# Kernel tuning notes

Measured on AMD Instinct MI355X. Metric: run time of the kernel, lower is better.

The kernel has to match this reference:

```python
import jax, jax.numpy as jnp
import numpy as np

B, T, DIM = 4, 1024, 1024
HEADS, DH = 16, 64
MEM, CMEM, RATIO = 1024, 256, 4
KV = CMEM + MEM + T  # 2304
TOTAL_MEM = MEM + CMEM  # 1280
NEG = -np.finfo(np.float32).max


def shift(x):
    # Faithful port of the pad/flatten/reshape relative-position shift trick.
    b, h, i, j = x.shape
    x = jnp.concatenate([x, jnp.zeros((b, h, i, i), x.dtype)], axis=-1)  # [b,h,i,i+j]
    l = i + j - 1
    x = x.reshape(b, h, i * (i + j))
    pad = (-x.shape[-1]) % l
    x = jnp.pad(x, ((0, 0), (0, 0), (0, pad)))
    x = x.reshape(b, h, -1, l)
    return x[:, :, :i, i - 1:]  # [b,h,i,j]


def setup_inputs() -> dict:
    key = jax.random.key(0)
    ks = jax.random.split(key, 10)
    s = 0.02
    return {
        "x": jax.random.normal(ks[0], (B, T, DIM), jnp.float32),
        "mem": jax.random.normal(ks[1], (B, MEM, DIM), jnp.float32),
        "cmem": jax.random.normal(ks[2], (B, CMEM, DIM), jnp.float32),
        "pos_emb": jax.random.normal(ks[3], (HEADS, KV, DH), jnp.float32),
        "input_mask": jnp.ones((B, T), bool),
        "Wq": jax.random.normal(ks[4], (DIM, DIM), jnp.float32) * s,
        "Wkv": jax.random.normal(ks[5], (2 * DIM, DIM), jnp.float32) * s,
        "Wout": jax.random.normal(ks[6], (DIM, DIM), jnp.float32) * s,
        "bout": jnp.zeros((DIM,), jnp.float32),
        "conv_w": jax.random.normal(ks[7], (DIM, DIM, RATIO), jnp.float32) * s,
        "conv_b": jnp.zeros((DIM,), jnp.float32),
    }


def reference(x, mem, cmem, pos_emb, input_mask, Wq, Wkv, Wout, bout, conv_w, conv_b):
    b, t, e = x.shape
    scale = DH ** -0.5

    q = x @ Wq.T                                             # [b,t,e]
    kv_input = jnp.concatenate([cmem, mem, x], axis=1)       # [b,kv,e]
    kv_len = kv_input.shape[1]
    kv = kv_input @ Wkv.T                                    # [b,kv,2e]
    k, v = jnp.split(kv, 2, axis=-1)

    def mh(z):
        return z.reshape(z.shape[0], z.shape[1], HEADS, DH).transpose(0, 2, 1, 3)

    qh, kh, vh = mh(q), mh(k), mh(v)                         # [b,h,*,dh]

    dots = jnp.einsum('bhid,bhjd->bhij', qh, kh) * scale     # [b,h,t,kv]

    pe = pos_emb[:, -kv_len:].astype(qh.dtype)               # [h,kv,dh]
    pos_dots = shift(jnp.einsum('bhid,hjd->bhij', qh, pe) * scale)
    dots = dots + pos_dots

    # input mask (padded True over mem+cmem positions)
    m = input_mask[:, None, :, None] & input_mask[:, None, None, :]  # [b,1,t,t]
    m = jnp.pad(m, ((0, 0), (0, 0), (0, 0), (TOTAL_MEM, 0)), constant_values=True)
    dots = jnp.where(m, dots, NEG)

    # causal mask shifted by total memory length
    causal = jnp.triu(jnp.ones((t, t + TOTAL_MEM), bool), k=1 + TOTAL_MEM)
    dots = jnp.where(causal[None, None], NEG, dots)

    attn = jax.nn.softmax(dots, axis=-1)
    out = jnp.einsum('bhij,bhjd->bhid', attn, vh)
    out = out.transpose(0, 2, 1, 3).reshape(b, t, e)
    logits = out @ Wout.T + bout

    # memory update (eval path, calc_memory=True)
    queue = jnp.concatenate([mem, x], axis=1)                # [b,mem+t,e]
    new_mem = queue[:, -MEM:]
    old_mem = jax.lax.stop_gradient(queue[:, :-MEM])         # [b,t,e], t % RATIO == 0
    comp = jax.lax.conv_general_dilated(
        old_mem.transpose(0, 2, 1), conv_w, (RATIO,), 'VALID',
        dimension_numbers=('NCH', 'OIH', 'NCH')) + conv_b[None, :, None]
    comp = comp.transpose(0, 2, 1)                           # [b,t//RATIO,e]
    new_cmem = jnp.concatenate([cmem, comp], axis=1)[:, -CMEM:]

    return logits, new_mem, new_cmem
```

## Files before the change

### kernel.cpp

```cpp
#include <hip/hip_runtime.h>
#include <hip/hip_bf16.h>
#include <hip/hip_fp16.h>
#include <cstdint>
#include <cstddef>
#include <cstring>

using bf16 = __hip_bfloat16;

constexpr int TS    = 1024;
constexpr int DIM   = 1024;
constexpr int MEMN  = 1024;
constexpr int CMEMN = 256;
constexpr int KVN   = 2304;
constexpr int TMEM  = 1280;

typedef __attribute__((ext_vector_type(8))) short short8;
typedef __attribute__((ext_vector_type(4))) float f32x4;

__device__ __forceinline__ unsigned short f2bf_us(float f){
    __hip_bfloat16 t = __float2bfloat16(f);
    unsigned short us; memcpy(&us, &t, 2); return us;
}
__device__ __forceinline__ int sw8(int row){ return (row & 7) ^ ((row >> 3) & 7); }

__device__ __forceinline__ short8 ldfrag(const unsigned short* base, int row, int chunk) {
    int ch = chunk ^ sw8(row);
    return *(const short8*)(base + row*64 + ch*8);
}
__device__ __forceinline__ void gl2lds16(const void* g, void* l) {
    __builtin_amdgcn_global_load_lds(
        (const __attribute__((address_space(1))) void*)g,
        (__attribute__((address_space(3))) void*)l, 16, 0, 0);
}
__device__ __forceinline__ short8 ldg8(const unsigned short* p){ return *(const short8*)p; }

__global__ __launch_bounds__(256) void pack(
    const float* __restrict__ x, const float* __restrict__ memp,
    const float* __restrict__ cmem, const float* __restrict__ Wq,
    const float* __restrict__ Wkv, const float* __restrict__ Wout,
    const float* __restrict__ cw, const float* __restrict__ pe,
    unsigned short* __restrict__ kvin, unsigned short* __restrict__ wqb,
    unsigned short* __restrict__ wkvb, unsigned short* __restrict__ woutb,
    unsigned short* __restrict__ cw2b, unsigned short* __restrict__ peb)
{
    const size_t t8 = ((size_t)blockIdx.x * 256 + threadIdx.x) * 8;
    unsigned short h[8];
    if (t8 < 9437184) {
        size_t g = t8 >> 10;
        int cc = (int)(t8 & 1023);
        int b = (int)(g / KVN), j = (int)(g % KVN);
        const float* src;
        if (j < CMEMN)      src = cmem + ((size_t)b*CMEMN + j)*1024 + cc;
        else if (j < TMEM)  src = memp + ((size_t)b*MEMN + (j - CMEMN))*1024 + cc;
        else                src = x    + ((size_t)b*TS   + (j - TMEM))*1024 + cc;
        float4 f0 = *(const float4*)src; float4 f1 = *(const float4*)(src + 4);
        h[0]=f2bf_us(f0.x); h[1]=f2bf_us(f0.y); h[2]=f2bf_us(f0.z); h[3]=f2bf_us(f0.w);
        h[4]=f2bf_us(f1.x); h[5]=f2bf_us(f1.y); h[6]=f2bf_us(f1.z); h[7]=f2bf_us(f1.w);
        *(uint4*)(kvin + t8) = *(const uint4*)h;
    } else if (t8 < 13631488) {
        const float* src; unsigned short* dst; float sc = 1.0f;
        if (t8 < 10485760)      { src = Wq   + (t8 - 9437184);  dst = wqb   + (t8 - 9437184); sc = 0.18033688011112043f; }
        else if (t8 < 12582912) { src = Wkv  + (t8 - 10485760); dst = wkvb  + (t8 - 10485760); }
        else                    { src = Wout + (t8 - 12582912); dst = woutb + (t8 - 12582912); }
        float4 f0 = *(const float4*)src; float4 f1 = *(const float4*)(src + 4);
        h[0]=f2bf_us(f0.x*sc); h[1]=f2bf_us(f0.y*sc); h[2]=f2bf_us(f0.z*sc); h[3]=f2bf_us(f0.w*sc);
        h[4]=f2bf_us(f1.x*sc); h[5]=f2bf_us(f1.y*sc); h[6]=f2bf_us(f1.z*sc); h[7]=f2bf_us(f1.w*sc);
        *(uint4*)dst = *(const uint4*)h;
    } else if (t8 < 17825792) {
        size_t o8 = t8 - 13631488;
        int o = (int)(o8 >> 12); int rem = (int)(o8 & 4095);
        int r = rem >> 10, i = rem & 1023;
        #pragma unroll
        for (int p = 0; p < 8; ++p) h[p] = f2bf_us(cw[(o << 12) + (i + p)*4 + r]);
        *(uint4*)(cw2b + o8) = *(const uint4*)h;
    } else {
        size_t o8 = t8 - 17825792;
        const float* src = pe + o8;
        float4 f0 = *(const float4*)src; float4 f1 = *(const float4*)(src + 4);
        h[0]=f2bf_us(f0.x); h[1]=f2bf_us(f0.y); h[2]=f2bf_us(f0.z); h[3]=f2bf_us(f0.w);
        h[4]=f2bf_us(f1.x); h[5]=f2bf_us(f1.y); h[6]=f2bf_us(f1.z); h[7]=f2bf_us(f1.w);
        *(uint4*)(peb + o8) = *(const uint4*)h;
    }
}

template<int EPI, int QMODE>
__global__ __launch_bounds__(256) void gemm_mfma(
    const bf16* __restrict__ Abf, const bf16* __restrict__ Bbf,
    const float* __restrict__ bias, void* __restrict__ Cptr,
    void* __restrict__ C2, int M, int N, int K)
{
    __shared__ alignas(16) unsigned short As[128*64];
    __shared__ alignas(16) unsigned short Bs[128*64];
    const int tid = threadIdx.x, lane = tid & 63, w = tid >> 6;
    const int quad = lane >> 4, colq = lane & 15;
    const int wm = w >> 1, wn = w & 1;
    const int m0 = blockIdx.x * 128, n0 = blockIdx.y * 128;
    size_t abase;
    if (QMODE == 0)      abase = (size_t)m0 * K;
    else if (QMODE == 1) abase = ((size_t)((m0 >> 10)*KVN + TMEM + (m0 & 1023))) * 1024;
    else                 abase = ((size_t)((m0 >> 8)*KVN + CMEMN)) * 1024 + (size_t)(m0 & 255) * 4096;
    const unsigned short* Ag = (const unsigned short*)Abf + abase;
    const unsigned short* Bg = (const unsigned short*)Bbf + (size_t)n0 * K;

    const int srow0 = w*32 + (lane >> 3);
    const int sch2  = lane & 7;

    f32x4 acc[4][4];
    #pragma unroll
    for (int i = 0; i < 4; ++i)
        #pragma unroll
        for (int j = 0; j < 4; ++j) acc[i][j] = (f32x4){0.f,0.f,0.f,0.f};

    for (int k0 = 0; k0 < K; k0 += 64) {
        __syncthreads();
        #pragma unroll
        for (int c = 0; c < 4; ++c) {
            int rr = srow0 + c*8;
            int ch = sch2 ^ sw8(rr);
            gl2lds16(Ag + (size_t)rr*K + k0 + ch*8, &As[(w*32 + c*8)*64]);
            gl2lds16(Bg + (size_t)rr*K + k0 + ch*8, &Bs[(w*32 + c*8)*64]);
        }
        __syncthreads();
        short8 af[4][2], bfr[4][2];
        #pragma unroll
        for (int i = 0; i < 4; ++i) {
            af[i][0]  = ldfrag(As, wm*64 + i*16 + colq, quad);
            af[i][1]  = ldfrag(As, wm*64 + i*16 + colq, 4 + quad);
            bfr[i][0] = ldfrag(Bs, wn*64 + i*16 + colq, quad);
            bfr[i][1] = ldfrag(Bs, wn*64 + i*16 + colq, 4 + quad);
        }
        #pragma unroll
        for (int i = 0; i < 4; ++i)
            #pragma unroll
            for (int j = 0; j < 4; ++j) {
                f32x4 t = __builtin_amdgcn_mfma_f32_16x16x32_bf16(af[i][0], bfr[j][0], acc[i][j], 0, 0, 0);
                acc[i][j] = __builtin_amdgcn_mfma_f32_16x16x32_bf16(af[i][1], bfr[j][1], t, 0, 0, 0);
            }
    }
    if (EPI == 2) {
        const int b = m0 / KVN;
        const int jj0 = (m0 - b*KVN) + wm*64;
        if (n0 < 1024) {
            bf16* kn = (bf16*)Cptr;
            #pragma unroll
            for (int j = 0; j < 4; ++j) {
                int col = n0 + wn*64 + j*16 + colq;
                #pragma unroll
                for (int i = 0; i < 4; ++i)
                    #pragma unroll
                    for (int r = 0; r < 4; ++r)
                        kn[(size_t)(b*KVN + jj0 + i*16 + quad*4 + r)*1024 + col] =
                            __float2bfloat16(acc[i][j][r]);
            }
        } else {
            unsigned short* vp = (unsigned short*)C2;
            #pragma unroll
            for (int j = 0; j < 4; ++j) {
                int col = n0 + wn*64 + j*16 + colq;
                int hh = (col >> 6) & 15, d = col & 63;
                #pragma unroll
                for (int i = 0; i < 4; ++i) {
                    int jjb = jj0 + i*16 + quad*4;
                    ushort4 u;
                    u.x = f2bf_us(acc[i][j][0]); u.y = f2bf_us(acc[i][j][1]);
                    u.z = f2bf_us(acc[i][j][2]); u.w = f2bf_us(acc[i][j][3]);
                    *(ushort4*)(vp + ((size_t)((b*16 + hh)*64 + d))*KVN + jjb) = u;
                }
            }
        }
    } else {
        #pragma unroll
        for (int j = 0; j < 4; ++j) {
            int col = n0 + wn*64 + j*16 + colq;
            float bj = bias ? bias[col] : 0.0f;
            #pragma unroll
            for (int i = 0; i < 4; ++i)
                #pragma unroll
                for (int r = 0; r < 4; ++r) {
                    size_t row = (size_t)(m0 + wm*64 + i*16 + quad*4 + r);
                    float v = acc[i][j][r] + bj;
                    if (EPI == 1) ((bf16*)Cptr)[row*N + col] = __float2bfloat16(v);
                    else          ((float*)Cptr)[row*N + col] = v;
                }
        }
    }
}

__global__ __launch_bounds__(256, 2) void attn(
    const unsigned short* __restrict__ qg,
    const unsigned short* __restrict__ kq,
    const unsigned short* __restrict__ vh,
    const unsigned short* __restrict__ peb,
    bf16* __restrict__ out)
{
    __shared__ alignas(16) unsigned short Kt[2][64*64];
    __shared__ alignas(16) unsigned short PEr[256*64];
    __shared__ alignas(16) unsigned short Pb[64*64];

    const int tid  = threadIdx.x;
    const int lane = tid & 63, w = tid >> 6;
    const int quad = lane >> 4, colq = lane & 15;
    const int jr = lane >> 3, l7 = lane & 7;

    const int bx = blockIdx.x;
    const int b = bx & 3, h = (bx >> 2) & 15;
    const int pp = bx >> 6;
    const int qt = (pp < 4) ? pp : 11 - pp;
    const int q0 = qt * 128;

    const unsigned short* kbase = kq  + (size_t)b*KVN*1024 + h*64;
    const unsigned short* vbase = vh  + ((size_t)((b*16 + h)*64))*KVN;
    const unsigned short* pbase = peb + (size_t)h*KVN*64;

    short8 qa[2][2];
    #pragma unroll
    for (int it2 = 0; it2 < 2; ++it2) {
        const unsigned short* qp = qg + ((size_t)(b*1024 + q0 + 32*w + 16*it2 + colq))*1024 + h*64;
        qa[it2][0] = ldg8(qp + quad*8);
        qa[it2][1] = ldg8(qp + 32 + quad*8);
    }
    __builtin_amdgcn_sched_barrier(0);

    const int row0 = w*8 + jr;
    const int row1 = 32 + row0;
    const int ch0 = (l7 ^ sw8(row0))*8;
    const int ch1 = (l7 ^ sw8(row1))*8;

    auto stage_k = [&](int kv0s, int buf) {
        gl2lds16(kbase + (size_t)(kv0s + row0)*1024 + ch0, &Kt[buf][(w*8)*64]);
        gl2lds16(kbase + (size_t)(kv0s + row1)*1024 + ch1, &Kt[buf][(32 + w*8)*64]);
    };
    auto stage_pe = [&](int cbase) {
        int cg0 = cbase + row0, cg1 = cbase + row1;
        gl2lds16(pbase + (size_t)min(cg0, KVN-1)*64 + (l7 ^ sw8(cg0 & 255))*8,
                 &PEr[((cbase + w*8) & 255)*64]);
        gl2lds16(pbase + (size_t)min(cg1, KVN-1)*64 + (l7 ^ sw8(cg1 & 255))*8,
                 &PEr[((cbase + 32 + w*8) & 255)*64]);
    };

    const int c0p = 896 - q0;
    #pragma unroll
    for (int c = 0; c < 4; ++c) {
        int cg = c0p + c*32 + w*8 + jr;
        gl2lds16(pbase + (size_t)cg*64 + (l7 ^ sw8(cg & 255))*8,
                 &PEr[((c0p + c*32 + w*8) & 255)*64]);
    }
    stage_pe(1024 - q0);
    stage_k(0, 0);
    stage_k(64, 1);
    __builtin_amdgcn_sched_barrier(0);

    f32x4 oacc[2][4];
    float l_[2][4];
    #pragma unroll
    for (int it2 = 0; it2 < 2; ++it2) {
        #pragma unroll
        for (int dt = 0; dt < 4; ++dt) oacc[it2][dt] = (f32x4){0.f,0.f,0.f,0.f};
        #pragma unroll
        for (int r = 0; r < 4; ++r) l_[it2][r] = 0.f;
    }
    const f32x4 zero4 = (f32x4){0.f,0.f,0.f,0.f};
    const int nkv = min(36, ((q0 + 1407) >> 6) + 1);
    int cur = 0;

    for (int kvt = 0; kvt < nkv; ++kvt) {
        const int kv0 = kvt * 64;
        short8 vf[4][2];
        #pragma unroll
        for (int dt = 0; dt < 4; ++dt) {
            const unsigned short* vp = vbase + (size_t)(dt*16 + colq)*KVN + kv0;
            vf[dt][0] = ldg8(vp + quad*8);
            vf[dt][1] = ldg8(vp + 32 + quad*8);
        }
        __builtin_amdgcn_sched_barrier(0);
        if (kvt == nkv - 1) { asm volatile("s_waitcnt vmcnt(8)" ::: "memory"); }
        else                { asm volatile("s_waitcnt vmcnt(10)" ::: "memory"); }
        __builtin_amdgcn_s_barrier();

        const unsigned short* KtC = &Kt[cur][0];
        short8 kf[4][2];
        #pragma unroll
        for (int nt = 0; nt < 4; ++nt) {
            kf[nt][0] = ldfrag(KtC, nt*16 + colq, quad);
            kf[nt][1] = ldfrag(KtC, nt*16 + colq, 4 + quad);
        }
        asm volatile("s_waitcnt lgkmcnt(0)" ::: "memory");
        __builtin_amdgcn_s_barrier();

        if (kvt + 1 < nkv) stage_pe(kv0 + 64 - q0 + 1024);
        if (kvt + 2 < nkv) stage_k(kv0 + 128, cur);
        __builtin_amdgcn_sched_barrier(0);

        f32x4 facc[2][4], pacc[2][5];
        __builtin_amdgcn_s_setprio(1);
        #pragma unroll
        for (int it2 = 0; it2 < 2; ++it2)
            #pragma unroll
            for (int nt = 0; nt < 4; ++nt) {
                f32x4 t = __builtin_amdgcn_mfma_f32_16x16x32_bf16(qa[it2][0], kf[nt][0], zero4, 0, 0, 0);
                facc[it2][nt] = __builtin_amdgcn_mfma_f32_16x16x32_bf16(qa[it2][1], kf[nt][1], t, 0, 0, 0);
            }
        #pragma unroll
        for (int it2 = 0; it2 < 2; ++it2) {
            const int cb = kv0 - q0 + 1008 - 32*w - 16*it2;
            #pragma unroll
            for (int pnt = 0; pnt < 5; ++pnt) {
                int slot = (cb + pnt*16 + colq) & 255;
                short8 b0 = ldfrag(PEr, slot, quad);
                short8 b1 = ldfrag(PEr, slot, 4 + quad);
                f32x4 t = __builtin_amdgcn_mfma_f32_16x16x32_bf16(qa[it2][0], b0, zero4, 0, 0, 0);
                pacc[it2][pnt] = __builtin_amdgcn_mfma_f32_16x16x32_bf16(qa[it2][1], b1, t, 0, 0, 0);
            }
        }
        __builtin_amdgcn_s_setprio(0);

        #pragma unroll
        for (int it2 = 0; it2 < 2; ++it2) {
            const int prow0 = 16*w + 4*quad;
            #pragma unroll
            for (int r = 0; r < 4; ++r) {
                int tt = colq + 15 - 4*quad - r;
                int src = (lane & 48) | (tt & 15);
                float sh[5];
                #pragma unroll
                for (int p = 0; p < 5; ++p) sh[p] = __shfl(pacc[it2][p][r], src, 64);
                int ig = q0 + 32*w + 16*it2 + 4*quad + r;
                float lsum = 0.f;
                float ps[4];
                #pragma unroll
                for (int nt = 0; nt < 4; ++nt) {
                    float g = (tt < 16) ? sh[nt] : sh[nt + 1];
                    float v = facc[it2][nt][r] + g;
                    int jg = kv0 + nt*16 + colq;
                    float s = (jg - ig > TMEM) ? -1e30f : v;
                    ps[nt] = __builtin_exp2f(s);
                    lsum += ps[nt];
                }
                l_[it2][r] += lsum;
                int prow = prow0 + r;
                int swp = sw8(prow);
                #pragma unroll
                for (int nt = 0; nt < 4; ++nt) {
                    int cc = nt*16 + colq;
                    Pb[prow*64 + (((cc >> 3) ^ swp))*8 + (cc & 7)] = f2bf_us(ps[nt]);
                }
            }
            short8 pa0 = ldfrag(Pb, 16*w + colq, quad);
            short8 pa1 = ldfrag(Pb, 16*w + colq, 4 + quad);
            __builtin_amdgcn_s_setprio(1);
            #pragma unroll
            for (int dt = 0; dt < 4; ++dt) {
                f32x4 t = __builtin_amdgcn_mfma_f32_16x16x32_bf16(pa0, vf[dt][0], oacc[it2][dt], 0, 0, 0);
                oacc[it2][dt] = __builtin_amdgcn_mfma_f32_16x16x32_bf16(pa1, vf[dt][1], t, 0, 0, 0);
            }
            __builtin_amdgcn_s_setprio(0);
        }
        cur ^= 1;
    }

    #pragma unroll
    for (int it2 = 0; it2 < 2; ++it2) {
        #pragma unroll
        for (int r = 0; r < 4; ++r) {
            float lt = l_[it2][r];
            #pragma unroll
            for (int off = 1; off < 16; off <<= 1) lt += __shfl_xor(lt, off, 64);
            float inv = 1.0f / lt;
            size_t row = (size_t)(b*1024 + q0 + 32*w + 16*it2 + 4*quad + r);
            #pragma unroll
            for (int dt = 0; dt < 4; ++dt)
                out[row*1024 + h*64 + dt*16 + colq] = __float2bfloat16(oacc[it2][dt][r] * inv);
        }
    }
}

__global__ __launch_bounds__(256) void copy_u4(const uint4* __restrict__ src,
                                               uint4* __restrict__ dst, int n)
{
    int i = blockIdx.x * 256 + threadIdx.x;
    if (i < n) dst[i] = src[i];
}

extern "C" void kernel_launch(void* const* d_in, const int* in_sizes, int n_in,
                              void* d_out, int out_size, void* d_ws, size_t ws_size,
                              hipStream_t stream)
{
    const float* x    = (const float*)d_in[0];
    const float* memp = (const float*)d_in[1];
    const float* cmem = (const float*)d_in[2];
    const float* pe   = (const float*)d_in[3];
    const float* Wq   = (const float*)d_in[5];
    const float* Wkv  = (const float*)d_in[6];
    const float* Wout = (const float*)d_in[7];
    const float* bout = (const float*)d_in[8];
    const float* cw   = (const float*)d_in[9];
    const float* cb   = (const float*)d_in[10];
    float* outp = (float*)d_out;

    char* wsb = (char*)d_ws;
    unsigned short* kvin  = (unsigned short*)(wsb);
    unsigned short* knat  = (unsigned short*)(wsb + 18874368);
    unsigned short* vhb   = (unsigned short*)(wsb + 37748736);
    unsigned short* qb    = (unsigned short*)(wsb + 56623104);
    bf16*           ao    = (bf16*)(wsb + 65011712);
    unsigned short* wqb   = (unsigned short*)(wsb + 73400320);
    unsigned short* wkvb  = (unsigned short*)(wsb + 75497472);
    unsigned short* woutb = (unsigned short*)(wsb + 79691776);
    unsigned short* cw2b  = (unsigned short*)(wsb + 81788928);
    unsigned short* peb   = (unsigned short*)(wsb + 90177536);

    pack<<<dim3(9856), 256, 0, stream>>>(x, memp, cmem, Wq, Wkv, Wout, cw, pe,
        kvin, wqb, wkvb, woutb, cw2b, peb);
    gemm_mfma<1,1><<<dim3(32, 8), 256, 0, stream>>>((const bf16*)kvin, (const bf16*)wqb,
        nullptr, qb, nullptr, 4096, 1024, 1024);
    gemm_mfma<2,0><<<dim3(72, 16), 256, 0, stream>>>((const bf16*)kvin, (const bf16*)wkvb,
        nullptr, knat, vhb, 9216, 2048, 1024);
    attn<<<dim3(512), 256, 0, stream>>>(qb, knat, vhb, peb, ao);
    gemm_mfma<0,0><<<dim3(32, 8), 256, 0, stream>>>(ao, (const bf16*)woutb,
        bout, outp, nullptr, 4096, 1024, 1024);
    copy_u4<<<dim3(4096), 256, 0, stream>>>((const uint4*)x,
        (uint4*)(outp + 4194304), 1048576);
    gemm_mfma<0,2><<<dim3(8, 8), 256, 0, stream>>>((const bf16*)kvin, (const bf16*)cw2b,
        cb, outp + 8388608, nullptr, 1024, 1024, 4096);
}
```

Before: 519.9 us.

## Templatize GEMM tile sizes and stage V-transpose epilogue through LDS

Measured after the change: 483.6 us. -7.0%, faster.

```diff
diff --git a/kernel.cpp b/kernel.cpp
--- a/kernel.cpp
+++ b/kernel.cpp
@@ -83,18 +83,25 @@
     }
 }
 
-template<int EPI, int QMODE>
+template<int EPI, int QMODE, int BM, int NB>
 __global__ __launch_bounds__(256) void gemm_mfma(
     const bf16* __restrict__ Abf, const bf16* __restrict__ Bbf,
     const float* __restrict__ bias, void* __restrict__ Cptr,
     void* __restrict__ C2, int M, int N, int K)
 {
-    __shared__ alignas(16) unsigned short As[128*64];
-    __shared__ alignas(16) unsigned short Bs[128*64];
+    constexpr int MI = (BM == 128) ? 4 : 2;
+    constexpr int NJ = (NB == 128) ? 4 : 2;
+    constexpr int WROWS = BM / 2;
+    constexpr int WCOLS = NB / 2;
+    __shared__ alignas(16) unsigned short Sh[(BM + NB) * 64];
+    unsigned short* As = Sh;
+    unsigned short* Bs = Sh + BM*64;
+
     const int tid = threadIdx.x, lane = tid & 63, w = tid >> 6;
     const int quad = lane >> 4, colq = lane & 15;
     const int wm = w >> 1, wn = w & 1;
-    const int m0 = blockIdx.x * 128, n0 = blockIdx.y * 128;
+    const int jr = lane >> 3, l7 = lane & 7;
+    const int m0 = blockIdx.x * BM, n0 = blockIdx.y * NB;
     size_t abase;
     if (QMODE == 0)      abase = (size_t)m0 * K;
     else if (QMODE == 1) abase = ((size_t)((m0 >> 10)*KVN + TMEM + (m0 & 1023))) * 1024;
@@ -102,82 +109,98 @@
     const unsigned short* Ag = (const unsigned short*)Abf + abase;
     const unsigned short* Bg = (const unsigned short*)Bbf + (size_t)n0 * K;
 
-    const int srow0 = w*32 + (lane >> 3);
-    const int sch2  = lane & 7;
-
-    f32x4 acc[4][4];
+    f32x4 acc[MI][NJ];
     #pragma unroll
-    for (int i = 0; i < 4; ++i)
-        #pragma unroll
-        for (int j = 0; j < 4; ++j) acc[i][j] = (f32x4){0.f,0.f,0.f,0.f};
+    for (int i = 0; i < MI; ++i)
+        #pragma unroll
+        for (int j = 0; j < NJ; ++j) acc[i][j] = (f32x4){0.f,0.f,0.f,0.f};
 
     for (int k0 = 0; k0 < K; k0 += 64) {
         __syncthreads();
         #pragma unroll
-        for (int c = 0; c < 4; ++c) {
-            int rr = srow0 + c*8;
-            int ch = sch2 ^ sw8(rr);
-            gl2lds16(Ag + (size_t)rr*K + k0 + ch*8, &As[(w*32 + c*8)*64]);
-            gl2lds16(Bg + (size_t)rr*K + k0 + ch*8, &Bs[(w*32 + c*8)*64]);
+        for (int c = 0; c < BM/32; ++c) {
+            int rr = w*(BM/4) + c*8 + jr;
+            int ch = l7 ^ sw8(rr);
+            gl2lds16(Ag + (size_t)rr*K + k0 + ch*8, &As[(w*(BM/4) + c*8)*64]);
+        }
+        #pragma unroll
+        for (int c = 0; c < NB/32; ++c) {
+            int rr = w*(NB/4) + c*8 + jr;
+            int ch = l7 ^ sw8(rr);
+            gl2lds16(Bg + (size_t)rr*K + k0 + ch*8, &Bs[(w*(NB/4) + c*8)*64]);
         }
         __syncthreads();
-        short8 af[4][2], bfr[4][2];
-        #pragma unroll
-        for (int i = 0; i < 4; ++i) {
-            af[i][0]  = ldfrag(As, wm*64 + i*16 + colq, quad);
-            af[i][1]  = ldfrag(As, wm*64 + i*16 + colq, 4 + quad);
-            bfr[i][0] = ldfrag(Bs, wn*64 + i*16 + colq, quad);
-            bfr[i][1] = ldfrag(Bs, wn*64 + i*16 + colq, 4 + quad);
-        }
-        #pragma unroll
-        for (int i = 0; i < 4; ++i)
-            #pragma unroll
-            for (int j = 0; j < 4; ++j) {
+        short8 af[MI][2], bfr[NJ][2];
+        #pragma unroll
+        for (int i = 0; i < MI; ++i) {
+            af[i][0]  = ldfrag(As, wm*WROWS + i*16 + colq, quad);
+            af[i][1]  = ldfrag(As, wm*WROWS + i*16 + colq, 4 + quad);
+        }
+        #pragma unroll
+        for (int j = 0; j < NJ; ++j) {
+            bfr[j][0] = ldfrag(Bs, wn*WCOLS + j*16 + colq, quad);
+            bfr[j][1] = ldfrag(Bs, wn*WCOLS + j*16 + colq, 4 + quad);
+        }
+        #pragma unroll
+        for (int i = 0; i < MI; ++i)
+            #pragma unroll
+            for (int j = 0; j < NJ; ++j) {
                 f32x4 t = __builtin_amdgcn_mfma_f32_16x16x32_bf16(af[i][0], bfr[j][0], acc[i][j], 0, 0, 0);
                 acc[i][j] = __builtin_amdgcn_mfma_f32_16x16x32_bf16(af[i][1], bfr[j][1], t, 0, 0, 0);
             }
     }
     if (EPI == 2) {
         const int b = m0 / KVN;
-        const int jj0 = (m0 - b*KVN) + wm*64;
+        const int jjbase = m0 - b*KVN;
         if (n0 < 1024) {
             bf16* kn = (bf16*)Cptr;
             #pragma unroll
-            for (int j = 0; j < 4; ++j) {
-                int col = n0 + wn*64 + j*16 + colq;
-                #pragma unroll
-                for (int i = 0; i < 4; ++i)
+            for (int j = 0; j < NJ; ++j) {
+                int col = n0 + wn*WCOLS + j*16 + colq;
+                #pragma unroll
+                for (int i = 0; i < MI; ++i)
                     #pragma unroll
                     for (int r = 0; r < 4; ++r)
-                        kn[(size_t)(b*KVN + jj0 + i*16 + quad*4 + r)*1024 + col] =
+                        kn[(size_t)(b*KVN + jjbase + wm*WROWS + i*16 + quad*4 + r)*1024 + col] =
                             __float2bfloat16(acc[i][j][r]);
             }
         } else {
-            unsigned short* vp = (unsigned short*)C2;
-            #pragma unroll
-            for (int j = 0; j < 4; ++j) {
-                int col = n0 + wn*64 + j*16 + colq;
-                int hh = (col >> 6) & 15, d = col & 63;
-                #pragma unroll
-                for (int i = 0; i < 4; ++i) {
-                    int jjb = jj0 + i*16 + quad*4;
-                    ushort4 u;
-                    u.x = f2bf_us(acc[i][j][0]); u.y = f2bf_us(acc[i][j][1]);
-                    u.z = f2bf_us(acc[i][j][2]); u.w = f2bf_us(acc[i][j][3]);
-                    *(ushort4*)(vp + ((size_t)((b*16 + hh)*64 + d))*KVN + jjb) = u;
+            unsigned short* T = Sh;
+            for (int p = 0; p < 2; ++p) {
+                __syncthreads();
+                if (wn == p) {
+                    #pragma unroll
+                    for (int j = 0; j < NJ; ++j) {
+                        int cl = j*16 + colq;
+                        #pragma unroll
+                        for (int i = 0; i < MI; ++i)
+                            #pragma unroll
+                            for (int r = 0; r < 4; ++r)
+                                T[cl*136 + wm*WROWS + i*16 + quad*4 + r] = f2bf_us(acc[i][j][r]);
+                    }
                 }
+                __syncthreads();
+                int hh = ((n0 + p*64) >> 6) & 15;
+                unsigned short* vp = (unsigned short*)C2 + ((size_t)(b*16 + hh)*64)*KVN;
+                #pragma unroll
+                for (int lp = 0; lp < 4; ++lp) {
+                    int idx = lp*256 + tid;
+                    int cl = idx >> 4, seg = idx & 15;
+                    short8 v = *(const short8*)(T + cl*136 + seg*8);
+                    *(short8*)(vp + (size_t)cl*KVN + jjbase + seg*8) = v;
+                }
             }
         }
     } else {
         #pragma unroll
-        for (int j = 0; j < 4; ++j) {
-            int col = n0 + wn*64 + j*16 + colq;
+        for (int j = 0; j < NJ; ++j) {
+            int col = n0 + wn*WCOLS + j*16 + colq;
             float bj = bias ? bias[col] : 0.0f;
             #pragma unroll
-            for (int i = 0; i < 4; ++i)
+            for (int i = 0; i < MI; ++i)
                 #pragma unroll
                 for (int r = 0; r < 4; ++r) {
-                    size_t row = (size_t)(m0 + wm*64 + i*16 + quad*4 + r);
+                    size_t row = (size_t)(m0 + wm*WROWS + i*16 + quad*4 + r);
                     float v = acc[i][j][r] + bj;
                     if (EPI == 1) ((bf16*)Cptr)[row*N + col] = __float2bfloat16(v);
                     else          ((float*)Cptr)[row*N + col] = v;
@@ -411,15 +434,15 @@
 
     pack<<<dim3(9856), 256, 0, stream>>>(x, memp, cmem, Wq, Wkv, Wout, cw, pe,
         kvin, wqb, wkvb, woutb, cw2b, peb);
-    gemm_mfma<1,1><<<dim3(32, 8), 256, 0, stream>>>((const bf16*)kvin, (const bf16*)wqb,
+    gemm_mfma<1,1,64,128><<<dim3(64, 8), 256, 0, stream>>>((const bf16*)kvin, (const bf16*)wqb,
         nullptr, qb, nullptr, 4096, 1024, 1024);
-    gemm_mfma<2,0><<<dim3(72, 16), 256, 0, stream>>>((const bf16*)kvin, (const bf16*)wkvb,
+    gemm_mfma<2,0,128,128><<<dim3(72, 16), 256, 0, stream>>>((const bf16*)kvin, (const bf16*)wkvb,
         nullptr, knat, vhb, 9216, 2048, 1024);
     attn<<<dim3(512), 256, 0, stream>>>(qb, knat, vhb, peb, ao);
-    gemm_mfma<0,0><<<dim3(32, 8), 256, 0, stream>>>(ao, (const bf16*)woutb,
+    gemm_mfma<0,0,64,128><<<dim3(64, 8), 256, 0, stream>>>(ao, (const bf16*)woutb,
         bout, outp, nullptr, 4096, 1024, 1024);
     copy_u4<<<dim3(4096), 256, 0, stream>>>((const uint4*)x,
         (uint4*)(outp + 4194304), 1048576);
-    gemm_mfma<0,2><<<dim3(8, 8), 256, 0, stream>>>((const bf16*)kvin, (const bf16*)cw2b,
+    gemm_mfma<0,2,64,64><<<dim3(16, 16), 256, 0, stream>>>((const bf16*)kvin, (const bf16*)cw2b,
         cb, outp + 8388608, nullptr, 1024, 1024, 4096);
 }
```
